# Kernel tuning notes

Hardware: AMD Instinct MI355X
Metric: run time of the kernel (lower is better)

## Reference

```python
import jax, jax.numpy as jnp
import numpy as np

EPS = 1e-12  # torch F.normalize default eps


def setup_inputs() -> dict:
    key = jax.random.key(0)
    k1, k2, k3, k4 = jax.random.split(key, 4)
    N, F_IN, F_OUT = 8192, 128, 128
    x = jax.random.normal(k1, (N, F_IN), dtype=jnp.float32)
    adj = jax.random.uniform(k2, (N, N), dtype=jnp.float32)
    # fc_layer params (xavier_uniform with relu gain for W, default-ish bias)
    gain = float(np.sqrt(2.0))
    limit = gain * float(np.sqrt(6.0 / (F_IN + F_OUT)))
    W = jax.random.uniform(k3, (F_OUT, F_IN), dtype=jnp.float32, minval=-limit, maxval=limit)
    b = jax.random.uniform(k4, (F_OUT,), dtype=jnp.float32, minval=-1.0 / np.sqrt(F_IN), maxval=1.0 / np.sqrt(F_IN))
    return {"x": x, "adj": adj, "W": W, "b": b}


def reference(x, adj, W, b):
    N = adj.shape[0]
    # A' = A + I (self loops)
    a = adj + jnp.eye(N, dtype=adj.dtype)
    # degree normalization D^-1/2 A' D^-1/2 as a fused broadcast scale
    # (the torch code does this via two dense diag matmuls; same math)
    dinv = jax.lax.rsqrt(jnp.sum(a, axis=-1))  # [N]
    a = a * dinv[:, None] * dinv[None, :]
    # aggregation + linear
    h = a @ x                    # [N, F_IN]
    h = h @ W.T + b              # [N, F_OUT]
    # F.normalize(dim=1): L2 normalize each row
    norm = jnp.linalg.norm(h, axis=1, keepdims=True)
    return h / jnp.maximum(norm, EPS)
```

## Files before the change

### kernel.cpp

```cpp
#include <hip/hip_runtime.h>
#include <hip/hip_bf16.h>


typedef __attribute__((ext_vector_type(8))) short short8;
typedef __attribute__((ext_vector_type(4))) float f32x4;
typedef __attribute__((ext_vector_type(4))) unsigned short us4;

static __device__ __forceinline__ unsigned short f2bf(float f) {
    unsigned int u = __float_as_uint(f);
    u += 0x7FFFu + ((u >> 16) & 1u);
    return (unsigned short)(u >> 16);
}

static __device__ __forceinline__ void gload16(const void* g, const void* l) {
    __builtin_amdgcn_global_load_lds(
        (const __attribute__((address_space(1))) unsigned int*)g,
        (__attribute__((address_space(3))) unsigned int*)l, 16, 0, 0);
}

__global__ __launch_bounds__(512) void gcn_prep(
    const float* __restrict__ adj, const float* __restrict__ x,
    const float* __restrict__ W,
    unsigned short* __restrict__ yT, float* __restrict__ dinv,
    unsigned short* __restrict__ Wb, unsigned short* __restrict__ adjb)
{
    const int tid = threadIdx.x;
    const int blk = blockIdx.x;
    if (blk >= 256) {
        int idx = (blk - 256) * 512 + tid;
        Wb[idx] = f2bf(W[idx]);
        return;
    }
    const int wave   = tid >> 6;
    const int lane   = tid & 63;
    const int rowsel = lane >> 4;
    const int l16    = lane & 15;
    const long j0 = (long)blk * 32;
    const long j  = j0 + wave * 4 + rowsel;
    const int rt = (int)(j >> 4);
    const int ln = (int)(j & 15);
    const int q  = (l16 >> 1) & 3;
    const int jj = (l16 & 1) * 4;

    __shared__ float s_di[32];

    const float4* rowp = (const float4*)(adj + j * 8192L);
    float s = 0.f;
#pragma unroll 8
    for (int it = 0; it < 128; ++it) {
        float4 v = rowp[it * 16 + l16];
        s += (v.x + v.y) + (v.z + v.w);
        int ks = it * 2 + (l16 >> 3);
        us4 w4;
        w4.x = f2bf(v.x); w4.y = f2bf(v.y);
        w4.z = f2bf(v.z); w4.w = f2bf(v.w);
        *(us4*)&adjb[(((long)rt * 256 + ks) * 64 + q * 16 + ln) * 8 + jj] = w4;
    }
    s += __shfl_xor(s, 1, 64);
    s += __shfl_xor(s, 2, 64);
    s += __shfl_xor(s, 4, 64);
    s += __shfl_xor(s, 8, 64);
    if (l16 == 0) s_di[wave * 4 + rowsel] = rsqrtf(s + 1.0f);
    __syncthreads();
    if (tid < 32) dinv[j0 + tid] = s_di[tid];

    const int jy = tid & 31;
    const int fb = tid >> 5;
    const float di = s_di[jy];
#pragma unroll
    for (int p = 0; p < 8; ++p) {
        int f = p * 16 + fb;
        yT[(long)f * 8192 + j0 + jy] = f2bf(di * x[(j0 + jy) * 128 + f]);
    }
}

#define CK 16
#define NCHUNK 16

__global__ __launch_bounds__(512) void gcn_main(
    const unsigned short* __restrict__ adjb, const float* __restrict__ x,
    const float* __restrict__ bias,
    const unsigned short* __restrict__ yT, const float* __restrict__ dinv,
    const unsigned short* __restrict__ Wb, float* __restrict__ out)
{
    __shared__ unsigned short AbS[2][32 * 512];

    const int tid  = threadIdx.x;
    const int wave = tid >> 6;
    const int lane = tid & 63;
    const int q    = lane >> 4;
    const int ln   = lane & 15;
    const int blk  = blockIdx.x;
    const long rowBase = (long)blk * 32;

    f32x4 acc[2] = {};

    auto stage = [&](int c, int buf) {
#pragma unroll
        for (int i = 0; i < 4; ++i) {
            int s = i * 8 + wave;
            const char* src = (const char*)adjb +
                ((((long)(blk * 2 + (s >> 4))) * 256 + c * CK + (s & 15)) * 64 + lane) * 16;
            gload16(src, &AbS[buf][s * 512]);
        }
    };

    stage(0, 0);
    __syncthreads();

    const unsigned short* bcol = &yT[(wave * 16 + ln) * 8192L + q * 8];

#pragma unroll 1
    for (int c = 0; c < NCHUNK; ++c) {
        const int cur = c & 1;
        if (c + 1 < NCHUNK) stage(c + 1, cur ^ 1);
#pragma unroll
        for (int ks = 0; ks < CK; ++ks) {
            short8 a0 = *(const short8*)&AbS[cur][ks * 512 + lane * 8];
            short8 a1 = *(const short8*)&AbS[cur][(16 + ks) * 512 + lane * 8];
            short8 b  = *(const short8*)&bcol[c * 512 + ks * 32];
            acc[0] = __builtin_amdgcn_mfma_f32_16x16x32_bf16(a0, b, acc[0], 0, 0, 0);
            acc[1] = __builtin_amdgcn_mfma_f32_16x16x32_bf16(a1, b, acc[1], 0, 0, 0);
        }
        __syncthreads();
    }

    unsigned short* t_lds = &AbS[0][0];
    float* s_dinv = (float*)(t_lds + 32 * 136);
    float* s_part = s_dinv + 32;
    float* s_inv  = s_part + 256;

    if (tid < 32) s_dinv[tid] = dinv[rowBase + tid];
    __syncthreads();

#pragma unroll
    for (int rt = 0; rt < 2; ++rt)
#pragma unroll
        for (int r = 0; r < 4; ++r) {
            int m = rt * 16 + q * 4 + r;
            int n = wave * 16 + ln;
            float di = s_dinv[m];
            float tv = di * acc[rt][r] + di * di * x[(rowBase + m) * 128 + n];
            t_lds[m * 136 + n] = f2bf(tv);
        }
    __syncthreads();

    f32x4 z[2] = {};
#pragma unroll
    for (int s = 0; s < 4; ++s) {
        const int k0 = s * 32 + q * 8;
        short8 a0 = *(const short8*)&t_lds[ln * 136 + k0];
        short8 a1 = *(const short8*)&t_lds[(16 + ln) * 136 + k0];
        short8 b  = *(const short8*)&Wb[(wave * 16 + ln) * 128 + k0];
        z[0] = __builtin_amdgcn_mfma_f32_16x16x32_bf16(a0, b, z[0], 0, 0, 0);
        z[1] = __builtin_amdgcn_mfma_f32_16x16x32_bf16(a1, b, z[1], 0, 0, 0);
    }

    float bv = bias[wave * 16 + ln];
    float zv[2][4], rp[2][4];
#pragma unroll
    for (int rt = 0; rt < 2; ++rt)
#pragma unroll
        for (int r = 0; r < 4; ++r) {
            float v = z[rt][r] + bv;
            zv[rt][r] = v;
            rp[rt][r] = v * v;
        }
#pragma unroll
    for (int rt = 0; rt < 2; ++rt)
#pragma unroll
        for (int r = 0; r < 4; ++r) {
            rp[rt][r] += __shfl_xor(rp[rt][r], 1, 64);
            rp[rt][r] += __shfl_xor(rp[rt][r], 2, 64);
            rp[rt][r] += __shfl_xor(rp[rt][r], 4, 64);
            rp[rt][r] += __shfl_xor(rp[rt][r], 8, 64);
        }
    if (ln == 0) {
#pragma unroll
        for (int rt = 0; rt < 2; ++rt)
#pragma unroll
            for (int r = 0; r < 4; ++r)
                s_part[(rt * 16 + q * 4 + r) * 8 + wave] = rp[rt][r];
    }
    __syncthreads();
    if (tid < 32) {
        float s = 0.f;
#pragma unroll
        for (int w = 0; w < 8; ++w) s += s_part[tid * 8 + w];
        s_inv[tid] = 1.0f / fmaxf(sqrtf(s), 1e-12f);
    }
    __syncthreads();

#pragma unroll
    for (int rt = 0; rt < 2; ++rt)
#pragma unroll
        for (int r = 0; r < 4; ++r) {
            int m = rt * 16 + q * 4 + r;
            out[(rowBase + m) * 128 + wave * 16 + ln] = zv[rt][r] * s_inv[m];
        }
}

extern "C" void kernel_launch(void* const* d_in, const int* in_sizes, int n_in,
                              void* d_out, int out_size, void* d_ws, size_t ws_size,
                              hipStream_t stream) {
    const float* x   = (const float*)d_in[0];
    const float* adj = (const float*)d_in[1];
    const float* W   = (const float*)d_in[2];
    const float* b   = (const float*)d_in[3];
    float* out = (float*)d_out;

    unsigned short* yT   = (unsigned short*)d_ws;
    float*          dv   = (float*)((char*)d_ws + (2u << 20));
    unsigned short* Wb   = (unsigned short*)((char*)d_ws + (2u << 20) + 32768);
    unsigned short* adjb = (unsigned short*)((char*)d_ws + (4u << 20));

    gcn_prep<<<256 + 32, 512, 0, stream>>>(adj, x, W, yT, dv, Wb, adjb);
    gcn_main<<<256, 512, 0, stream>>>(adjb, x, b, yT, dv, Wb, out);
}
```

Measured before the change: 459.4 us.

## Fuse prep and main kernels into one cooperative launch with grid sync

Merges the adjacency conversion/degree kernel and the aggregation GEMM kernel into a single cooperative kernel separated by a grid-wide barrier. Each block keeps its own row degrees in shared memory instead of writing them to global memory and reading them back. This removes one kernel launch and the gap between launches. The cost is a grid sync and the cooperative-launch residency requirement of 256 blocks of 512 threads.

```diff
diff --git a/kernel.cpp b/kernel.cpp
--- a/kernel.cpp
+++ b/kernel.cpp
@@ -1,5 +1,8 @@
 #include <hip/hip_runtime.h>
 #include <hip/hip_bf16.h>
+#include <hip/hip_cooperative_groups.h>
+
+namespace cg = cooperative_groups;
 
 
 typedef __attribute__((ext_vector_type(8))) short short8;
@@ -18,80 +21,70 @@
         (__attribute__((address_space(3))) unsigned int*)l, 16, 0, 0);
 }
 
-__global__ __launch_bounds__(512) void gcn_prep(
-    const float* __restrict__ adj, const float* __restrict__ x,
-    const float* __restrict__ W,
-    unsigned short* __restrict__ yT, float* __restrict__ dinv,
-    unsigned short* __restrict__ Wb, unsigned short* __restrict__ adjb)
-{
-    const int tid = threadIdx.x;
-    const int blk = blockIdx.x;
-    if (blk >= 256) {
-        int idx = (blk - 256) * 512 + tid;
-        Wb[idx] = f2bf(W[idx]);
-        return;
-    }
-    const int wave   = tid >> 6;
-    const int lane   = tid & 63;
-    const int rowsel = lane >> 4;
-    const int l16    = lane & 15;
-    const long j0 = (long)blk * 32;
-    const long j  = j0 + wave * 4 + rowsel;
-    const int rt = (int)(j >> 4);
-    const int ln = (int)(j & 15);
-    const int q  = (l16 >> 1) & 3;
-    const int jj = (l16 & 1) * 4;
-
-    __shared__ float s_di[32];
-
-    const float4* rowp = (const float4*)(adj + j * 8192L);
-    float s = 0.f;
-#pragma unroll 8
-    for (int it = 0; it < 128; ++it) {
-        float4 v = rowp[it * 16 + l16];
-        s += (v.x + v.y) + (v.z + v.w);
-        int ks = it * 2 + (l16 >> 3);
-        us4 w4;
-        w4.x = f2bf(v.x); w4.y = f2bf(v.y);
-        w4.z = f2bf(v.z); w4.w = f2bf(v.w);
-        *(us4*)&adjb[(((long)rt * 256 + ks) * 64 + q * 16 + ln) * 8 + jj] = w4;
-    }
-    s += __shfl_xor(s, 1, 64);
-    s += __shfl_xor(s, 2, 64);
-    s += __shfl_xor(s, 4, 64);
-    s += __shfl_xor(s, 8, 64);
-    if (l16 == 0) s_di[wave * 4 + rowsel] = rsqrtf(s + 1.0f);
-    __syncthreads();
-    if (tid < 32) dinv[j0 + tid] = s_di[tid];
-
-    const int jy = tid & 31;
-    const int fb = tid >> 5;
-    const float di = s_di[jy];
-#pragma unroll
-    for (int p = 0; p < 8; ++p) {
-        int f = p * 16 + fb;
-        yT[(long)f * 8192 + j0 + jy] = f2bf(di * x[(j0 + jy) * 128 + f]);
-    }
-}
-
 #define CK 16
 #define NCHUNK 16
 
-__global__ __launch_bounds__(512) void gcn_main(
-    const unsigned short* __restrict__ adjb, const float* __restrict__ x,
-    const float* __restrict__ bias,
-    const unsigned short* __restrict__ yT, const float* __restrict__ dinv,
-    const unsigned short* __restrict__ Wb, float* __restrict__ out)
+__global__ __launch_bounds__(512) void gcn_fused(
+    const float* __restrict__ adj, const float* __restrict__ x,
+    const float* __restrict__ W, const float* __restrict__ bias,
+    unsigned short* __restrict__ yT, unsigned short* __restrict__ Wb,
+    unsigned short* __restrict__ adjb, float* __restrict__ out)
 {
     __shared__ unsigned short AbS[2][32 * 512];
+    __shared__ float s_di[32];
 
     const int tid  = threadIdx.x;
+    const int blk  = blockIdx.x;
     const int wave = tid >> 6;
     const int lane = tid & 63;
-    const int q    = lane >> 4;
-    const int ln   = lane & 15;
-    const int blk  = blockIdx.x;
     const long rowBase = (long)blk * 32;
+
+    {
+        const int rowsel = lane >> 4;
+        const int l16    = lane & 15;
+        const long j = rowBase + wave * 4 + rowsel;
+        const int rt = (int)(j >> 4);
+        const int ln = (int)(j & 15);
+        const int q  = (l16 >> 1) & 3;
+        const int jj = (l16 & 1) * 4;
+
+        const float4* rowp = (const float4*)(adj + j * 8192L);
+        float s = 0.f;
+#pragma unroll 8
+        for (int it = 0; it < 128; ++it) {
+            float4 v = rowp[it * 16 + l16];
+            s += (v.x + v.y) + (v.z + v.w);
+            int ks = it * 2 + (l16 >> 3);
+            us4 w4;
+            w4.x = f2bf(v.x); w4.y = f2bf(v.y);
+            w4.z = f2bf(v.z); w4.w = f2bf(v.w);
+            *(us4*)&adjb[(((long)rt * 256 + ks) * 64 + q * 16 + ln) * 8 + jj] = w4;
+        }
+        s += __shfl_xor(s, 1, 64);
+        s += __shfl_xor(s, 2, 64);
+        s += __shfl_xor(s, 4, 64);
+        s += __shfl_xor(s, 8, 64);
+        if (l16 == 0) s_di[wave * 4 + rowsel] = rsqrtf(s + 1.0f);
+        __syncthreads();
+
+        const int jy = tid & 31;
+        const int fb = tid >> 5;
+        const float di = s_di[jy];
+#pragma unroll
+        for (int p = 0; p < 8; ++p) {
+            int f = p * 16 + fb;
+            yT[(long)f * 8192 + rowBase + jy] = f2bf(di * x[(rowBase + jy) * 128 + f]);
+        }
+        if (blk < 32) {
+            int idx = blk * 512 + tid;
+            Wb[idx] = f2bf(W[idx]);
+        }
+    }
+
+    cg::this_grid().sync();
+
+    const int q  = lane >> 4;
+    const int ln = lane & 15;
 
     f32x4 acc[2] = {};
 
@@ -126,12 +119,8 @@
     }
 
     unsigned short* t_lds = &AbS[0][0];
-    float* s_dinv = (float*)(t_lds + 32 * 136);
-    float* s_part = s_dinv + 32;
+    float* s_part = (float*)(t_lds + 32 * 136);
     float* s_inv  = s_part + 256;
-
-    if (tid < 32) s_dinv[tid] = dinv[rowBase + tid];
-    __syncthreads();
 
 #pragma unroll
     for (int rt = 0; rt < 2; ++rt)
@@ -139,7 +128,7 @@
         for (int r = 0; r < 4; ++r) {
             int m = rt * 16 + q * 4 + r;
             int n = wave * 16 + ln;
-            float di = s_dinv[m];
+            float di = s_di[m];
             float tv = di * acc[rt][r] + di * di * x[(rowBase + m) * 128 + n];
             t_lds[m * 136 + n] = f2bf(tv);
         }
@@ -210,10 +199,13 @@
     float* out = (float*)d_out;
 
     unsigned short* yT   = (unsigned short*)d_ws;
-    float*          dv   = (float*)((char*)d_ws + (2u << 20));
     unsigned short* Wb   = (unsigned short*)((char*)d_ws + (2u << 20) + 32768);
     unsigned short* adjb = (unsigned short*)((char*)d_ws + (4u << 20));
 
-    gcn_prep<<<256 + 32, 512, 0, stream>>>(adj, x, W, yT, dv, Wb, adjb);
-    gcn_main<<<256, 512, 0, stream>>>(adjb, x, b, yT, dv, Wb, out);
-}
+    void* args[] = {
+        (void*)&adj, (void*)&x, (void*)&W, (void*)&b,
+        (void*)&yT, (void*)&Wb, (void*)&adjb, (void*)&out
+    };
+    hipLaunchCooperativeKernel((const void*)gcn_fused, dim3(256), dim3(512),
+                               args, 0, stream);
+}
```

New measurement: 504.5 us. 9.8% more time.

## Halve rows per block to 16 and batch adjacency loads in prep

Applied to the files above, without the earlier changes.

Both kernels now handle 16 rows per block instead of 32, doubling the grid to 512 blocks so more of the MI355X's compute units stay busy. The prep kernel reads each adjacency row with 32 lanes and issues eight float4 loads before converting, which raises memory-level parallelism for the dominant 256 MB fp32 read. The main kernel now does one MFMA per k-step instead of two, so each yT B-operand fetch is reused over half as many rows. That doubles total yT traffic, traded against better occupancy and load balance.

```diff
diff --git a/kernel.cpp b/kernel.cpp
--- a/kernel.cpp
+++ b/kernel.cpp
@@ -26,51 +26,60 @@
 {
     const int tid = threadIdx.x;
     const int blk = blockIdx.x;
-    if (blk >= 256) {
-        int idx = (blk - 256) * 512 + tid;
+    if (blk >= 512) {
+        int idx = (blk - 512) * 512 + tid;
         Wb[idx] = f2bf(W[idx]);
         return;
     }
-    const int wave   = tid >> 6;
-    const int lane   = tid & 63;
-    const int rowsel = lane >> 4;
-    const int l16    = lane & 15;
-    const long j0 = (long)blk * 32;
-    const long j  = j0 + wave * 4 + rowsel;
-    const int rt = (int)(j >> 4);
-    const int ln = (int)(j & 15);
-    const int q  = (l16 >> 1) & 3;
-    const int jj = (l16 & 1) * 4;
-
-    __shared__ float s_di[32];
-
-    const float4* rowp = (const float4*)(adj + j * 8192L);
+    const int wave = tid >> 6;
+    const int lane = tid & 63;
+    const int half = lane >> 5;
+    const int l32  = lane & 31;
+    const long j0  = (long)blk * 16;
+    const long row = j0 + wave * 2 + half;
+    const int rt = (int)(row >> 4);
+    const int ln = (int)(row & 15);
+    const int q  = (l32 & 7) >> 1;
+    const int jj = (l32 & 1) * 4;
+
+    __shared__ float s_di[16];
+
+    const float4* rowp = (const float4*)(adj + row * 8192L);
     float s = 0.f;
-#pragma unroll 8
-    for (int it = 0; it < 128; ++it) {
-        float4 v = rowp[it * 16 + l16];
-        s += (v.x + v.y) + (v.z + v.w);
-        int ks = it * 2 + (l16 >> 3);
-        us4 w4;
-        w4.x = f2bf(v.x); w4.y = f2bf(v.y);
-        w4.z = f2bf(v.z); w4.w = f2bf(v.w);
-        *(us4*)&adjb[(((long)rt * 256 + ks) * 64 + q * 16 + ln) * 8 + jj] = w4;
+#pragma unroll 1
+    for (int bt = 0; bt < 8; ++bt) {
+        float4 st[8];
+#pragma unroll
+        for (int i = 0; i < 8; ++i)
+            st[i] = rowp[(bt * 8 + i) * 32 + l32];
+#pragma unroll
+        for (int i = 0; i < 8; ++i) {
+            float4 v = st[i];
+            s += (v.x + v.y) + (v.z + v.w);
+            int it = bt * 8 + i;
+            int ks = it * 4 + (l32 >> 3);
+            us4 w4;
+            w4.x = f2bf(v.x); w4.y = f2bf(v.y);
+            w4.z = f2bf(v.z); w4.w = f2bf(v.w);
+            *(us4*)&adjb[(((long)rt * 256 + ks) * 64 + q * 16 + ln) * 8 + jj] = w4;
+        }
     }
     s += __shfl_xor(s, 1, 64);
     s += __shfl_xor(s, 2, 64);
     s += __shfl_xor(s, 4, 64);
     s += __shfl_xor(s, 8, 64);
-    if (l16 == 0) s_di[wave * 4 + rowsel] = rsqrtf(s + 1.0f);
-    __syncthreads();
-    if (tid < 32) dinv[j0 + tid] = s_di[tid];
-
-    const int jy = tid & 31;
-    const int fb = tid >> 5;
+    s += __shfl_xor(s, 16, 64);
+    if (l32 == 0) s_di[wave * 2 + half] = rsqrtf(s + 1.0f);
+    __syncthreads();
+    if (tid < 16) dinv[j0 + tid] = s_di[tid];
+
+    const int jy = tid & 15;
+    const int f0 = tid >> 4;
     const float di = s_di[jy];
 #pragma unroll
-    for (int p = 0; p < 8; ++p) {
-        int f = p * 16 + fb;
-        yT[(long)f * 8192 + j0 + jy] = f2bf(di * x[(j0 + jy) * 128 + f]);
+    for (int p = 0; p < 4; ++p) {
+        int f = p * 32 + f0;
+        yT[(long)f * 8192 + j0 + jy] = f2bf(di * x[(int)(j0 + jy) * 128 + f]);
     }
 }
 
@@ -83,7 +92,7 @@
     const unsigned short* __restrict__ yT, const float* __restrict__ dinv,
     const unsigned short* __restrict__ Wb, float* __restrict__ out)
 {
-    __shared__ unsigned short AbS[2][32 * 512];
+    __shared__ unsigned short AbS[2][16 * 512];
 
     const int tid  = threadIdx.x;
     const int wave = tid >> 6;
@@ -91,16 +100,16 @@
     const int q    = lane >> 4;
     const int ln   = lane & 15;
     const int blk  = blockIdx.x;
-    const long rowBase = (long)blk * 32;
-
-    f32x4 acc[2] = {};
+    const long rowBase = (long)blk * 16;
+
+    f32x4 acc = {};
 
     auto stage = [&](int c, int buf) {
 #pragma unroll
-        for (int i = 0; i < 4; ++i) {
-            int s = i * 8 + wave;
+        for (int i = 0; i < 2; ++i) {
+            int s = wave * 2 + i;
             const char* src = (const char*)adjb +
-                ((((long)(blk * 2 + (s >> 4))) * 256 + c * CK + (s & 15)) * 64 + lane) * 16;
+                (((long)blk * 256 + c * CK + s) * 64 + lane) * 16;
             gload16(src, &AbS[buf][s * 512]);
         }
     };
@@ -116,74 +125,62 @@
         if (c + 1 < NCHUNK) stage(c + 1, cur ^ 1);
 #pragma unroll
         for (int ks = 0; ks < CK; ++ks) {
-            short8 a0 = *(const short8*)&AbS[cur][ks * 512 + lane * 8];
-            short8 a1 = *(const short8*)&AbS[cur][(16 + ks) * 512 + lane * 8];
-            short8 b  = *(const short8*)&bcol[c * 512 + ks * 32];
-            acc[0] = __builtin_amdgcn_mfma_f32_16x16x32_bf16(a0, b, acc[0], 0, 0, 0);
-            acc[1] = __builtin_amdgcn_mfma_f32_16x16x32_bf16(a1, b, acc[1], 0, 0, 0);
+            short8 a = *(const short8*)&AbS[cur][ks * 512 + lane * 8];
+            short8 b = *(const short8*)&bcol[c * 512 + ks * 32];
+            acc = __builtin_amdgcn_mfma_f32_16x16x32_bf16(a, b, acc, 0, 0, 0);
         }
         __syncthreads();
     }
 
     unsigned short* t_lds = &AbS[0][0];
-    float* s_dinv = (float*)(t_lds + 32 * 136);
-    float* s_part = s_dinv + 32;
-    float* s_inv  = s_part + 256;
-
-    if (tid < 32) s_dinv[tid] = dinv[rowBase + tid];
-    __syncthreads();
-
-#pragma unroll
-    for (int rt = 0; rt < 2; ++rt)
-#pragma unroll
-        for (int r = 0; r < 4; ++r) {
-            int m = rt * 16 + q * 4 + r;
-            int n = wave * 16 + ln;
-            float di = s_dinv[m];
-            float tv = di * acc[rt][r] + di * di * x[(rowBase + m) * 128 + n];
-            t_lds[m * 136 + n] = f2bf(tv);
-        }
-    __syncthreads();
-
-    f32x4 z[2] = {};
+    float* s_dinv = (float*)(t_lds + 16 * 136);
+    float* s_part = s_dinv + 16;
+    float* s_inv  = s_part + 128;
+
+    if (tid < 16) s_dinv[tid] = dinv[rowBase + tid];
+    __syncthreads();
+
+#pragma unroll
+    for (int r = 0; r < 4; ++r) {
+        int m = q * 4 + r;
+        int n = wave * 16 + ln;
+        float di = s_dinv[m];
+        float tv = di * acc[r] + di * di * x[(int)(rowBase + m) * 128 + n];
+        t_lds[m * 136 + n] = f2bf(tv);
+    }
+    __syncthreads();
+
+    f32x4 z = {};
 #pragma unroll
     for (int s = 0; s < 4; ++s) {
         const int k0 = s * 32 + q * 8;
-        short8 a0 = *(const short8*)&t_lds[ln * 136 + k0];
-        short8 a1 = *(const short8*)&t_lds[(16 + ln) * 136 + k0];
-        short8 b  = *(const short8*)&Wb[(wave * 16 + ln) * 128 + k0];
-        z[0] = __builtin_amdgcn_mfma_f32_16x16x32_bf16(a0, b, z[0], 0, 0, 0);
-        z[1] = __builtin_amdgcn_mfma_f32_16x16x32_bf16(a1, b, z[1], 0, 0, 0);
+        short8 a = *(const short8*)&t_lds[ln * 136 + k0];
+        short8 b = *(const short8*)&Wb[(wave * 16 + ln) * 128 + k0];
+        z = __builtin_amdgcn_mfma_f32_16x16x32_bf16(a, b, z, 0, 0, 0);
     }
 
     float bv = bias[wave * 16 + ln];
-    float zv[2][4], rp[2][4];
-#pragma unroll
-    for (int rt = 0; rt < 2; ++rt)
-#pragma unroll
-        for (int r = 0; r < 4; ++r) {
-            float v = z[rt][r] + bv;
-            zv[rt][r] = v;
-            rp[rt][r] = v * v;
-        }
-#pragma unroll
-    for (int rt = 0; rt < 2; ++rt)
-#pragma unroll
-        for (int r = 0; r < 4; ++r) {
-            rp[rt][r] += __shfl_xor(rp[rt][r], 1, 64);
-            rp[rt][r] += __shfl_xor(rp[rt][r], 2, 64);
-            rp[rt][r] += __shfl_xor(rp[rt][r], 4, 64);
-            rp[rt][r] += __shfl_xor(rp[rt][r], 8, 64);
-        }
+    float zv[4], rp[4];
+#pragma unroll
+    for (int r = 0; r < 4; ++r) {
+        float v = z[r] + bv;
+        zv[r] = v;
+        rp[r] = v * v;
+    }
+#pragma unroll
+    for (int r = 0; r < 4; ++r) {
+        rp[r] += __shfl_xor(rp[r], 1, 64);
+        rp[r] += __shfl_xor(rp[r], 2, 64);
+        rp[r] += __shfl_xor(rp[r], 4, 64);
+        rp[r] += __shfl_xor(rp[r], 8, 64);
+    }
     if (ln == 0) {
 #pragma unroll
-        for (int rt = 0; rt < 2; ++rt)
-#pragma unroll
-            for (int r = 0; r < 4; ++r)
-                s_part[(rt * 16 + q * 4 + r) * 8 + wave] = rp[rt][r];
-    }
-    __syncthreads();
-    if (tid < 32) {
+        for (int r = 0; r < 4; ++r)
+            s_part[(q * 4 + r) * 8 + wave] = rp[r];
+    }
+    __syncthreads();
+    if (tid < 16) {
         float s = 0.f;
 #pragma unroll
         for (int w = 0; w < 8; ++w) s += s_part[tid * 8 + w];
@@ -192,12 +189,10 @@
     __syncthreads();
 
 #pragma unroll
-    for (int rt = 0; rt < 2; ++rt)
-#pragma unroll
-        for (int r = 0; r < 4; ++r) {
-            int m = rt * 16 + q * 4 + r;
-            out[(rowBase + m) * 128 + wave * 16 + ln] = zv[rt][r] * s_inv[m];
-        }
+    for (int r = 0; r < 4; ++r) {
+        int m = q * 4 + r;
+        out[(int)(rowBase + m) * 128 + wave * 16 + ln] = zv[r] * s_inv[m];
+    }
 }
 
 extern "C" void kernel_launch(void* const* d_in, const int* in_sizes, int n_in,
@@ -214,6 +209,6 @@
     unsigned short* Wb   = (unsigned short*)((char*)d_ws + (2u << 20) + 32768);
     unsigned short* adjb = (unsigned short*)((char*)d_ws + (4u << 20));
 
-    gcn_prep<<<256 + 32, 512, 0, stream>>>(adj, x, W, yT, dv, Wb, adjb);
-    gcn_main<<<256, 512, 0, stream>>>(adjb, x, b, yT, dv, Wb, out);
-}
+    gcn_prep<<<512 + 32, 512, 0, stream>>>(adj, x, W, yT, dv, Wb, adjb);
+    gcn_main<<<512, 512, 0, stream>>>(adjb, x, b, yT, dv, Wb, out);
+}
```

Measured after the change: 515.1 us. 12.1% more time.

## Split adjacency row scan across two half-waves groups and batch loads in prep

Applied to the files above, without the earlier changes.

The prep kernel now processes 16 rows per block instead of 32, with two groups of four waves each covering half of every row, and the grid doubles to 512 row blocks. Partial row sums are combined through shared memory before the rsqrt. The row loop also issues eight float4 loads before converting and storing them, which puts more memory requests in flight. Together these aim to raise memory-level parallelism and occupancy in the bandwidth-bound 256MB adjacency read and bf16 conversion, at the cost of an extra barrier and a smaller yT transpose tile per block.

```diff
diff --git a/kernel.cpp b/kernel.cpp
--- a/kernel.cpp
+++ b/kernel.cpp
@@ -26,50 +26,66 @@
 {
     const int tid = threadIdx.x;
     const int blk = blockIdx.x;
-    if (blk >= 256) {
-        int idx = (blk - 256) * 512 + tid;
+    if (blk >= 512) {
+        int idx = (blk - 512) * 512 + tid;
         Wb[idx] = f2bf(W[idx]);
         return;
     }
     const int wave   = tid >> 6;
     const int lane   = tid & 63;
+    const int wq     = wave & 3;
+    const int h      = wave >> 2;
     const int rowsel = lane >> 4;
     const int l16    = lane & 15;
-    const long j0 = (long)blk * 32;
-    const long j  = j0 + wave * 4 + rowsel;
-    const int rt = (int)(j >> 4);
-    const int ln = (int)(j & 15);
+    const long j0  = (long)blk * 16;
+    const long row = j0 + wq * 4 + rowsel;
+    const int rt = (int)(row >> 4);
+    const int ln = (int)(row & 15);
     const int q  = (l16 >> 1) & 3;
     const int jj = (l16 & 1) * 4;
 
-    __shared__ float s_di[32];
-
-    const float4* rowp = (const float4*)(adj + j * 8192L);
+    __shared__ float s_half[16][2];
+    __shared__ float s_di[16];
+
+    const float4* rowp = (const float4*)(adj + row * 8192L) + (long)h * 1024;
     float s = 0.f;
-#pragma unroll 8
-    for (int it = 0; it < 128; ++it) {
-        float4 v = rowp[it * 16 + l16];
-        s += (v.x + v.y) + (v.z + v.w);
-        int ks = it * 2 + (l16 >> 3);
-        us4 w4;
-        w4.x = f2bf(v.x); w4.y = f2bf(v.y);
-        w4.z = f2bf(v.z); w4.w = f2bf(v.w);
-        *(us4*)&adjb[(((long)rt * 256 + ks) * 64 + q * 16 + ln) * 8 + jj] = w4;
+#pragma unroll 1
+    for (int bt = 0; bt < 8; ++bt) {
+        float4 st[8];
+#pragma unroll
+        for (int i = 0; i < 8; ++i)
+            st[i] = rowp[(bt * 8 + i) * 16 + l16];
+#pragma unroll
+        for (int i = 0; i < 8; ++i) {
+            float4 v = st[i];
+            s += (v.x + v.y) + (v.z + v.w);
+            int it = bt * 8 + i;
+            int ks = h * 128 + it * 2 + (l16 >> 3);
+            us4 w4;
+            w4.x = f2bf(v.x); w4.y = f2bf(v.y);
+            w4.z = f2bf(v.z); w4.w = f2bf(v.w);
+            *(us4*)&adjb[(((long)rt * 256 + ks) * 64 + q * 16 + ln) * 8 + jj] = w4;
+        }
     }
     s += __shfl_xor(s, 1, 64);
     s += __shfl_xor(s, 2, 64);
     s += __shfl_xor(s, 4, 64);
     s += __shfl_xor(s, 8, 64);
-    if (l16 == 0) s_di[wave * 4 + rowsel] = rsqrtf(s + 1.0f);
-    __syncthreads();
-    if (tid < 32) dinv[j0 + tid] = s_di[tid];
-
-    const int jy = tid & 31;
-    const int fb = tid >> 5;
+    if (l16 == 0) s_half[wq * 4 + rowsel][h] = s;
+    __syncthreads();
+    if (tid < 16) {
+        float di = rsqrtf(s_half[tid][0] + s_half[tid][1] + 1.0f);
+        dinv[j0 + tid] = di;
+        s_di[tid] = di;
+    }
+    __syncthreads();
+
+    const int jy = tid & 15;
+    const int f0 = tid >> 4;
     const float di = s_di[jy];
 #pragma unroll
-    for (int p = 0; p < 8; ++p) {
-        int f = p * 16 + fb;
+    for (int p = 0; p < 4; ++p) {
+        int f = p * 32 + f0;
         yT[(long)f * 8192 + j0 + jy] = f2bf(di * x[(j0 + jy) * 128 + f]);
     }
 }
@@ -214,6 +230,6 @@
     unsigned short* Wb   = (unsigned short*)((char*)d_ws + (2u << 20) + 32768);
     unsigned short* adjb = (unsigned short*)((char*)d_ws + (4u << 20));
 
-    gcn_prep<<<256 + 32, 512, 0, stream>>>(adj, x, W, yT, dv, Wb, adjb);
+    gcn_prep<<<512 + 32, 512, 0, stream>>>(adj, x, W, yT, dv, Wb, adjb);
     gcn_main<<<256, 512, 0, stream>>>(adjb, x, b, yT, dv, Wb, out);
 }
```

New measurement: 468.4 us. No clear change (+2.0%).
